# Optimization experiments

Hardware: AMD Instinct MI355X
Metric: run time of the kernel (lower is better)

Reference implementation:

```python
import jax, jax.numpy as jnp
import numpy as np

PI = 3.141592653589793


def setup_inputs() -> dict:
    key = jax.random.key(0)
    k1, k2, k3, k4 = jax.random.split(key, 4)
    B, N, C, H, V = 4, 4096, 128, 8, 16
    inputs = jax.random.normal(k1, (B, N, C), dtype=jnp.float32)
    dist = jax.random.uniform(k2, (N, N), dtype=jnp.float32)
    r = jax.random.normal(k3, (H, 1, 1), dtype=jnp.float32)
    weight = jax.random.normal(k4, (H, C, V), dtype=jnp.float32)
    return {"inputs": inputs, "dist": dist, "r": r, "weight": weight, "locality": 64}


def reference(inputs, dist, r, weight, locality):
    # scaled_dist: (H, N, N) -- learnable bandwidth per head via tan/sin transform
    scaled = dist[None, :, :] * jnp.tan(0.25 * PI * (1.0 + jnp.sin(r)))
    # quantile-based local masking along last axis (linear interpolation,
    # matching tfp.stats.percentile with interpolation='linear')
    mask = jnp.percentile(scaled, float(locality), axis=-1, keepdims=True, method="linear")
    fmax = jnp.finfo(jnp.float32).max
    scaled = jnp.where(scaled <= mask, scaled, fmax)
    # softmax over key axis of -scaled_dist (masked entries -> -fmax -> ~0 weight)
    att = jax.nn.softmax(-scaled, axis=-1)  # (H, N, N)
    # per-head value projection: (B,N,C) x (H,C,V) -> (B,H,N,V)
    value = jnp.einsum("bnj,hjk->bhnk", inputs, weight)
    # attention aggregation: (H,N,N) x (B,H,N,V) -> (B,H,N,V)
    concat = jnp.einsum("hnj,bhjd->bhnd", att, value)
    B, H, N, V = concat.shape
    concat = concat.transpose(0, 2, 1, 3).reshape(B, N, H * V)  # (B, N, hid_dim)
    # tf.keras.activations.gelu defaults to exact (non-approximate) gelu
    return jax.nn.gelu(concat, approximate=False)
```

## Files before the change

### kernel.cpp

```cpp
#include <hip/hip_runtime.h>
#include <hip/hip_bf16.h>
#include <math.h>

#define NN 4096
#define NC 128
#define NH 8
#define NV 16
#define NB 4
#define BD 64

typedef _Float16 half8 __attribute__((ext_vector_type(8)));
typedef float floatx4 __attribute__((ext_vector_type(4)));

__device__ __forceinline__ int get_loc(const int* locp){
    int lr = locp[0];
    return (lr >= 0 && lr <= 100) ? lr : 64;
}
__device__ __forceinline__ float head_scale(const float* rr, int h){
    float ts = tanf(0.78539816339744831f * (1.0f + sinf(rr[h])));
    if (!(ts > 0.f)) ts = (ts == 0.f) ? 1e-20f : 1e20f;
    if (ts > 1e20f) ts = 1e20f;
    return ts;
}
__device__ __forceinline__ void lds_barrier(){
    __asm__ __volatile__("s_waitcnt lgkmcnt(0)\n\ts_barrier" ::: "memory");
}

__global__ __launch_bounds__(256) void k_rowstats(const float* __restrict__ dist,
                                                  const int* __restrict__ locp,
                                                  float* __restrict__ Kval,
                                                  float* __restrict__ xminp){
    __shared__ unsigned int hist[4][256];
    __shared__ float cand[1024];
    __shared__ unsigned int cnt, selb_s, basec_s, xminu;
    const int i = blockIdx.x, t = threadIdx.x;
    const int wv = t >> 6, lane = t & 63;
    const int loc = get_loc(locp);
    const unsigned int rank = (unsigned int)(((long long)loc * (NN - 1)) / 100) + 1u;

    float v[16];
    const float4* rp = (const float4*)(dist + (size_t)i * NN);
#pragma unroll
    for (int k = 0; k < 4; k++){
        float4 x4 = rp[k * 256 + t];
        v[4*k+0] = x4.x; v[4*k+1] = x4.y; v[4*k+2] = x4.z; v[4*k+3] = x4.w;
    }
    for (int k = t; k < 1024; k += 256) ((unsigned int*)hist)[k] = 0;
    if (t == 0){ cnt = 0; selb_s = 255u; basec_s = 0u; xminu = 0xFFFFFFFFu; }
    __syncthreads();

    float lmin = 1e30f;
#pragma unroll
    for (int u = 0; u < 16; u++){
        float x = v[u];
        lmin = fminf(lmin, x);
        int b = (int)(x * 256.0f); b = b < 0 ? 0 : (b > 255 ? 255 : b);
        atomicAdd(&hist[wv][b], 1u);
    }
#pragma unroll
    for (int off = 1; off < 64; off <<= 1) lmin = fminf(lmin, __shfl_xor(lmin, off));
    if (lane == 0) atomicMin(&xminu, __float_as_uint(lmin));
    __syncthreads();

    if (t < 64){
        unsigned int lp[4];
        unsigned int run = 0;
#pragma unroll
        for (int q = 0; q < 4; q++){
            int b = 4 * t + q;
            run += hist[0][b] + hist[1][b] + hist[2][b] + hist[3][b];
            lp[q] = run;
        }
        unsigned int incl = run;
#pragma unroll
        for (int d = 1; d < 64; d <<= 1){
            unsigned int y = __shfl_up(incl, d);
            if (t >= d) incl += y;
        }
        unsigned int excl = incl - run;
        if (excl < rank && rank <= incl){
#pragma unroll
            for (int q = 0; q < 4; q++){
                if (excl + lp[q] >= rank){
                    selb_s  = (unsigned int)(4 * t + q);
                    basec_s = excl + (q ? lp[q-1] : 0u);
                    break;
                }
            }
        }
    }
    __syncthreads();
    const unsigned int sb = selb_s;
    if (t == 0) Kval[i] = ((float)sb + 1.0f) * 0.00390625f;
#pragma unroll
    for (int u = 0; u < 16; u++){
        float x = v[u];
        int b = (int)(x * 256.0f); b = b < 0 ? 0 : (b > 255 ? 255 : b);
        if ((unsigned int)b == sb){
            unsigned int idx = atomicAdd(&cnt, 1u);
            if (idx < 1024u) cand[idx] = x;
        }
    }
    __syncthreads();
    const unsigned int n = cnt > 1024u ? 1024u : cnt;
    const unsigned int need = rank - basec_s;
    for (unsigned int c0 = t; c0 < n; c0 += 256){
        float x = cand[c0];
        unsigned int lt = 0, le = 0;
        for (unsigned int k2 = 0; k2 < n; k2++){
            float y = cand[k2];
            lt += (y < x); le += (y <= x);
        }
        if (lt < need && need <= le) Kval[i] = x;
    }
    if (t == 0) xminp[i] = __uint_as_float(xminu);
}

__global__ __launch_bounds__(256) void k_value(const float* __restrict__ in,
                                               const float* __restrict__ wgt,
                                               _Float16* __restrict__ val_t){
    __shared__ float insh[NC * 65];
    __shared__ float wsh[NC * NV];
    const int j0 = blockIdx.x * 16;
    const int h  = blockIdx.y;
    const int t  = threadIdx.x;

    for (int k = t; k < NC * NV; k += 256) wsh[k] = wgt[h * NC * NV + k];
#pragma unroll
    for (int k = 0; k < 32; k++){
        int idx = k * 256 + t;
        int p = idx >> 7, c = idx & 127;
        int b = p >> 4, jl = p & 15;
        insh[c * 65 + jl * 4 + b] = in[((size_t)b * NN + j0 + jl) * NC + c];
    }
    __syncthreads();

    const int r = t & 63, dq = t >> 6;
    const int jl = r >> 2, b = r & 3;
    float a0 = 0.f, a1 = 0.f, a2 = 0.f, a3 = 0.f;
#pragma unroll 8
    for (int c = 0; c < NC; c++){
        float x = insh[c * 65 + r];
        float4 w4 = *(const float4*)&wsh[c * NV + dq * 4];
        a0 = fmaf(x, w4.x, a0);
        a1 = fmaf(x, w4.y, a1);
        a2 = fmaf(x, w4.z, a2);
        a3 = fmaf(x, w4.w, a3);
    }
    const size_t base = ((size_t)(h * BD + b * NV + dq * 4)) * NN + j0 + jl;
    val_t[base         ] = (_Float16)a0;
    val_t[base + NN    ] = (_Float16)a1;
    val_t[base + 2 * NN] = (_Float16)a2;
    val_t[base + 3 * NN] = (_Float16)a3;
}

__global__ __launch_bounds__(256) void k_att(const float* __restrict__ dist,
                                             const float* __restrict__ rr,
                                             const _Float16* __restrict__ val_t,
                                             const float* __restrict__ Kvalp,
                                             const float* __restrict__ xminp,
                                             float* __restrict__ out){
    __shared__ alignas(16) _Float16 wtile[2][32 * 72];
    __shared__ alignas(16) _Float16 vtile[2][64 * 72];

    const int i0 = blockIdx.x * 32;
    const int h  = blockIdx.y;
    const int t  = threadIdx.x;
    const int lane = t & 63, wv = t >> 6;
    const float ts  = head_scale(rr, h);
    const float ts2 = ts * 1.44269504088896f;

    const int il = t >> 3, jq = t & 7;
    const int vrow = t >> 3, vpart = t & 7;
    const float kvi  = Kvalp[i0 + il];
    const float txmi = ts2 * xminp[i0 + il];
    const float nts2 = -ts2;

    const float* dp = dist + (size_t)(i0 + il) * NN + jq * 8;
    const _Float16* vp0 = val_t + (size_t)(h * BD + vrow) * NN + vpart * 8;
    const _Float16* vp1 = vp0 + (size_t)32 * NN;

    half8 ones;
#pragma unroll
    for (int u = 0; u < 8; u++) ones[u] = (_Float16)1.0f;

    floatx4 acc0 = (floatx4){0.f,0.f,0.f,0.f};
    floatx4 acc1 = (floatx4){0.f,0.f,0.f,0.f};
    floatx4 accs = (floatx4){0.f,0.f,0.f,0.f};

    const int is16 = (wv & 1) * 16;
    const int bh   = (wv >> 1) * 32;
    const int aoff  = (is16 + (lane & 15)) * 72 + (lane >> 4) * 8;
    const int boff0 = (bh + (lane & 15)) * 72 + (lane >> 4) * 8;
    const int boff1 = boff0 + 16 * 72;
    const int voff0 = vrow * 72 + vpart * 8;
    const int voff1 = (vrow + 32) * 72 + vpart * 8;
    const int woff  = il * 72 + jq * 8;

    uint4 pv0 = *(const uint4*)vp0;  vp0 += 64;
    uint4 pv1 = *(const uint4*)vp1;  vp1 += 64;
    float4 pd0 = *(const float4*)dp;
    float4 pd1 = *(const float4*)(dp + 4);  dp += 64;

    {
        *(uint4*)&vtile[0][voff0] = pv0;
        *(uint4*)&vtile[0][voff1] = pv1;
        const float dd[8] = {pd0.x,pd0.y,pd0.z,pd0.w,pd1.x,pd1.y,pd1.z,pd1.w};
        half8 hw;
#pragma unroll
        for (int u = 0; u < 8; u++){
            float e = __builtin_amdgcn_exp2f(fmaf(nts2, dd[u], txmi));
            hw[u] = (_Float16)((dd[u] <= kvi) ? e : 0.f);
        }
        *(half8*)&wtile[0][woff] = hw;
    }

    for (int jt = 0; jt < NN / 64; jt++){
        const int cur = jt & 1;
        const bool more = (jt != NN / 64 - 1);
        if (more){
            pv0 = *(const uint4*)vp0;  vp0 += 64;
            pv1 = *(const uint4*)vp1;  vp1 += 64;
            pd0 = *(const float4*)dp;
            pd1 = *(const float4*)(dp + 4);  dp += 64;
        }
        lds_barrier();

#pragma unroll
        for (int kc = 0; kc < 2; kc++){
            half8 af = *(const half8*)&wtile[cur][aoff + kc * 32];
            half8 b0 = *(const half8*)&vtile[cur][boff0 + kc * 32];
            half8 b1 = *(const half8*)&vtile[cur][boff1 + kc * 32];
            acc0 = __builtin_amdgcn_mfma_f32_16x16x32_f16(af, b0, acc0, 0, 0, 0);
            acc1 = __builtin_amdgcn_mfma_f32_16x16x32_f16(af, b1, acc1, 0, 0, 0);
            accs = __builtin_amdgcn_mfma_f32_16x16x32_f16(af, ones, accs, 0, 0, 0);
        }

        if (more){
            const int nxt = 1 - cur;
            *(uint4*)&vtile[nxt][voff0] = pv0;
            *(uint4*)&vtile[nxt][voff1] = pv1;
            const float dd[8] = {pd0.x,pd0.y,pd0.z,pd0.w,pd1.x,pd1.y,pd1.z,pd1.w};
            half8 hw;
#pragma unroll
            for (int u = 0; u < 8; u++){
                float e = __builtin_amdgcn_exp2f(fmaf(nts2, dd[u], txmi));
                hw[u] = (_Float16)((dd[u] <= kvi) ? e : 0.f);
            }
            *(half8*)&wtile[nxt][woff] = hw;
        }
    }

    const int m0 = (lane >> 4) * 4;
    const int d  = lane & 15;
#pragma unroll
    for (int r4 = 0; r4 < 4; r4++){
        const int iloc = is16 + m0 + r4;
        const float inv_s = 1.0f / fmaxf(accs[r4], 1e-30f);
#pragma unroll
        for (int nt = 0; nt < 2; nt++){
            const int b = (wv >> 1) * 2 + nt;
            float c = acc0[r4], c1 = acc1[r4];
            float cc = (nt == 0 ? c : c1) * inv_s;
            float g = 0.5f * cc * (1.0f + erff(cc * 0.70710678118654752f));
            out[((size_t)b * NN + i0 + iloc) * (NH * NV) + h * NV + d] = g;
        }
    }
}

extern "C" void kernel_launch(void* const* d_in, const int* in_sizes, int n_in,
                              void* d_out, int out_size, void* d_ws, size_t ws_size,
                              hipStream_t stream) {
    const float* in   = (const float*)d_in[0];
    const float* dist = (const float*)d_in[1];
    const float* r    = (const float*)d_in[2];
    const float* wgt  = (const float*)d_in[3];
    const int*   loc  = (const int*)d_in[4];
    float* out = (float*)d_out;

    float* Kval = (float*)d_ws;
    float* xmin = Kval + NN;
    _Float16* val_t = (_Float16*)((char*)d_ws + 2 * (size_t)NN * sizeof(float));

    k_rowstats<<<NN, 256, 0, stream>>>(dist, loc, Kval, xmin);
    k_value<<<dim3(NN / 16, NH), 256, 0, stream>>>(in, wgt, val_t);
    k_att<<<dim3(NN / 32, NH), 256, 0, stream>>>(dist, r, val_t, Kval, xmin, out);
}
```

Measured before the change: 186.2 us.

## Split attention over batch halves and coalesce value-projection stores via LDS

k_att now launches a third grid dimension of two, each block handling 32 of the 64 batch-value columns. That halves the value tile in LDS and the accumulators per wave, and the launch bound is raised to ask for 8 blocks per CU. The trade-off is that the dist reads, the exp weight computation and the row-sum MFMA are duplicated across the two z-blocks. k_value now stages its fp16 outputs in shared memory and writes them as 8-byte stores, replacing scattered 2-byte global stores.

```diff
diff --git a/kernel.cpp b/kernel.cpp
--- a/kernel.cpp
+++ b/kernel.cpp
@@ -121,6 +121,7 @@
                                                _Float16* __restrict__ val_t){
     __shared__ float insh[NC * 65];
     __shared__ float wsh[NC * NV];
+    __shared__ _Float16 vout[64 * 20];
     const int j0 = blockIdx.x * 16;
     const int h  = blockIdx.y;
     const int t  = threadIdx.x;
@@ -147,24 +148,30 @@
         a2 = fmaf(x, w4.z, a2);
         a3 = fmaf(x, w4.w, a3);
     }
-    const size_t base = ((size_t)(h * BD + b * NV + dq * 4)) * NN + j0 + jl;
-    val_t[base         ] = (_Float16)a0;
-    val_t[base + NN    ] = (_Float16)a1;
-    val_t[base + 2 * NN] = (_Float16)a2;
-    val_t[base + 3 * NN] = (_Float16)a3;
-}
-
-__global__ __launch_bounds__(256) void k_att(const float* __restrict__ dist,
-                                             const float* __restrict__ rr,
-                                             const _Float16* __restrict__ val_t,
-                                             const float* __restrict__ Kvalp,
-                                             const float* __restrict__ xminp,
-                                             float* __restrict__ out){
+    const int row0 = b * NV + dq * 4;
+    vout[(row0    ) * 20 + jl] = (_Float16)a0;
+    vout[(row0 + 1) * 20 + jl] = (_Float16)a1;
+    vout[(row0 + 2) * 20 + jl] = (_Float16)a2;
+    vout[(row0 + 3) * 20 + jl] = (_Float16)a3;
+    __syncthreads();
+
+    const int row = t >> 2, part = t & 3;
+    *(uint2*)&val_t[((size_t)(h * BD + row)) * NN + j0 + part * 4] =
+        *(const uint2*)&vout[row * 20 + part * 4];
+}
+
+__global__ __launch_bounds__(256, 8) void k_att(const float* __restrict__ dist,
+                                                const float* __restrict__ rr,
+                                                const _Float16* __restrict__ val_t,
+                                                const float* __restrict__ Kvalp,
+                                                const float* __restrict__ xminp,
+                                                float* __restrict__ out){
     __shared__ alignas(16) _Float16 wtile[2][32 * 72];
-    __shared__ alignas(16) _Float16 vtile[2][64 * 72];
+    __shared__ alignas(16) _Float16 vtile[2][32 * 72];
 
     const int i0 = blockIdx.x * 32;
     const int h  = blockIdx.y;
+    const int bz = blockIdx.z;
     const int t  = threadIdx.x;
     const int lane = t & 63, wv = t >> 6;
     const float ts  = head_scale(rr, h);
@@ -177,34 +184,27 @@
     const float nts2 = -ts2;
 
     const float* dp = dist + (size_t)(i0 + il) * NN + jq * 8;
-    const _Float16* vp0 = val_t + (size_t)(h * BD + vrow) * NN + vpart * 8;
-    const _Float16* vp1 = vp0 + (size_t)32 * NN;
+    const _Float16* vp = val_t + (size_t)(h * BD + bz * 32 + vrow) * NN + vpart * 8;
 
     half8 ones;
 #pragma unroll
     for (int u = 0; u < 8; u++) ones[u] = (_Float16)1.0f;
 
-    floatx4 acc0 = (floatx4){0.f,0.f,0.f,0.f};
-    floatx4 acc1 = (floatx4){0.f,0.f,0.f,0.f};
+    floatx4 acc  = (floatx4){0.f,0.f,0.f,0.f};
     floatx4 accs = (floatx4){0.f,0.f,0.f,0.f};
 
     const int is16 = (wv & 1) * 16;
-    const int bh   = (wv >> 1) * 32;
-    const int aoff  = (is16 + (lane & 15)) * 72 + (lane >> 4) * 8;
-    const int boff0 = (bh + (lane & 15)) * 72 + (lane >> 4) * 8;
-    const int boff1 = boff0 + 16 * 72;
-    const int voff0 = vrow * 72 + vpart * 8;
-    const int voff1 = (vrow + 32) * 72 + vpart * 8;
-    const int woff  = il * 72 + jq * 8;
-
-    uint4 pv0 = *(const uint4*)vp0;  vp0 += 64;
-    uint4 pv1 = *(const uint4*)vp1;  vp1 += 64;
+    const int bq   = (wv >> 1) * 16;
+    const int aoff = (is16 + (lane & 15)) * 72 + (lane >> 4) * 8;
+    const int boff = (bq   + (lane & 15)) * 72 + (lane >> 4) * 8;
+    const int voff = vrow * 72 + vpart * 8;
+    const int woff = il * 72 + jq * 8;
+
+    uint4  pv  = *(const uint4*)vp;  vp += 64;
     float4 pd0 = *(const float4*)dp;
     float4 pd1 = *(const float4*)(dp + 4);  dp += 64;
-
     {
-        *(uint4*)&vtile[0][voff0] = pv0;
-        *(uint4*)&vtile[0][voff1] = pv1;
+        *(uint4*)&vtile[0][voff] = pv;
         const float dd[8] = {pd0.x,pd0.y,pd0.z,pd0.w,pd1.x,pd1.y,pd1.z,pd1.w};
         half8 hw;
 #pragma unroll
@@ -219,8 +219,7 @@
         const int cur = jt & 1;
         const bool more = (jt != NN / 64 - 1);
         if (more){
-            pv0 = *(const uint4*)vp0;  vp0 += 64;
-            pv1 = *(const uint4*)vp1;  vp1 += 64;
+            pv  = *(const uint4*)vp;  vp += 64;
             pd0 = *(const float4*)dp;
             pd1 = *(const float4*)(dp + 4);  dp += 64;
         }
@@ -229,17 +228,14 @@
 #pragma unroll
         for (int kc = 0; kc < 2; kc++){
             half8 af = *(const half8*)&wtile[cur][aoff + kc * 32];
-            half8 b0 = *(const half8*)&vtile[cur][boff0 + kc * 32];
-            half8 b1 = *(const half8*)&vtile[cur][boff1 + kc * 32];
-            acc0 = __builtin_amdgcn_mfma_f32_16x16x32_f16(af, b0, acc0, 0, 0, 0);
-            acc1 = __builtin_amdgcn_mfma_f32_16x16x32_f16(af, b1, acc1, 0, 0, 0);
+            half8 bf = *(const half8*)&vtile[cur][boff + kc * 32];
+            acc  = __builtin_amdgcn_mfma_f32_16x16x32_f16(af, bf,   acc,  0, 0, 0);
             accs = __builtin_amdgcn_mfma_f32_16x16x32_f16(af, ones, accs, 0, 0, 0);
         }
 
         if (more){
             const int nxt = 1 - cur;
-            *(uint4*)&vtile[nxt][voff0] = pv0;
-            *(uint4*)&vtile[nxt][voff1] = pv1;
+            *(uint4*)&vtile[nxt][voff] = pv;
             const float dd[8] = {pd0.x,pd0.y,pd0.z,pd0.w,pd1.x,pd1.y,pd1.z,pd1.w};
             half8 hw;
 #pragma unroll
@@ -252,19 +248,16 @@
     }
 
     const int m0 = (lane >> 4) * 4;
-    const int d  = lane & 15;
+    const int n  = lane & 15;
+    const int bd = bz * 32 + bq + n;
+    const int b  = bd >> 4, d = bd & 15;
 #pragma unroll
     for (int r4 = 0; r4 < 4; r4++){
         const int iloc = is16 + m0 + r4;
         const float inv_s = 1.0f / fmaxf(accs[r4], 1e-30f);
-#pragma unroll
-        for (int nt = 0; nt < 2; nt++){
-            const int b = (wv >> 1) * 2 + nt;
-            float c = acc0[r4], c1 = acc1[r4];
-            float cc = (nt == 0 ? c : c1) * inv_s;
-            float g = 0.5f * cc * (1.0f + erff(cc * 0.70710678118654752f));
-            out[((size_t)b * NN + i0 + iloc) * (NH * NV) + h * NV + d] = g;
-        }
+        float c = acc[r4] * inv_s;
+        float g = 0.5f * c * (1.0f + erff(c * 0.70710678118654752f));
+        out[((size_t)b * NN + i0 + iloc) * (NH * NV) + h * NV + d] = g;
     }
 }
 
@@ -284,5 +277,5 @@
 
     k_rowstats<<<NN, 256, 0, stream>>>(dist, loc, Kval, xmin);
     k_value<<<dim3(NN / 16, NH), 256, 0, stream>>>(in, wgt, val_t);
-    k_att<<<dim3(NN / 32, NH), 256, 0, stream>>>(dist, r, val_t, Kval, xmin, out);
-}
+    k_att<<<dim3(NN / 32, NH, 2), 256, 0, stream>>>(dist, r, val_t, Kval, xmin, out);
+}
```

Measured after the change: 219.0 us. 17.6% more time.
